# Optimization experiments

Measured on AMD Instinct MI355X. Metric: run time of the kernel, lower is better.

Reference implementation:

```python
import jax, jax.numpy as jnp
import numpy as np

B, S, D = 4, 1024, 1024
H = 16
DH = D // H  # head dim = 64
SCALE = DH ** -0.5
NEG = -1e18


def setup_inputs() -> dict:
    key = jax.random.key(0)
    ks = jax.random.split(key, 8)
    queries = jax.random.normal(ks[0], (B, S, D), dtype=jnp.float32)
    keys_ = jax.random.normal(ks[1], (B, S, D), dtype=jnp.float32)
    values = jax.random.normal(ks[2], (B, S, D), dtype=jnp.float32)
    mask = jax.random.randint(ks[3], (B, 1, S), 0, 2).astype(bool)
    sd = 1.0 / np.sqrt(D)
    Wq = jax.random.normal(ks[4], (D, D), dtype=jnp.float32) * sd
    Wk = jax.random.normal(ks[5], (D, D), dtype=jnp.float32) * sd
    Wv = jax.random.normal(ks[6], (D, D), dtype=jnp.float32) * sd
    Wo = jax.random.normal(ks[7], (D, D), dtype=jnp.float32) * sd
    return {"queries": queries, "keys": keys_, "values": values,
            "Wq": Wq, "Wk": Wk, "Wv": Wv, "Wo": Wo, "mask": mask}


def _split_heads(x):
    # [B,S,D] -> [B,H,S,DH]
    b, s, d = x.shape
    return x.reshape(b, s, H, d // H).transpose(0, 2, 1, 3)


def reference(queries, keys, values, Wq, Wk, Wv, Wo, mask):
    q = _split_heads(queries @ Wq) * SCALE          # [B,H,S,DH]
    k = _split_heads(keys @ Wk)                     # [B,H,S,DH]
    v = _split_heads(values @ Wv)                   # [B,H,S,DH]
    logits = jnp.einsum('bhqd,bhkd->bhqk', q, k)    # [B,H,S,S]
    # mask [B,1,Lk] -> unsqueeze head dim -> broadcast over [B,H,Lq,Lk]
    logits = jnp.where(mask[:, None, :, :], NEG, logits)
    attention_weights = logits.sum(axis=1) / H      # [B,S,S] head-averaged logits
    w = jax.nn.softmax(logits, axis=-1)             # dropout p=0 -> identity
    ctx = jnp.einsum('bhqk,bhkd->bhqd', w, v)       # [B,H,S,DH]
    ctx = ctx.transpose(0, 2, 1, 3).reshape(q.shape[0], q.shape[2], H * DH)
    outputs = ctx @ Wo                              # [B,S,D]
    return (outputs, attention_weights)
```

## Files before the change

### kernel.cpp

```cpp
#include <hip/hip_runtime.h>
#include <hip/hip_bf16.h>

typedef __bf16 bf16;
typedef __attribute__((ext_vector_type(8))) __bf16 bf16x8;
typedef __attribute__((ext_vector_type(4))) __bf16 bf16x4;
typedef __attribute__((ext_vector_type(4))) float f32x4;

#define NEGV (-1e18f)
#define LOG2E 1.4426950408889634f

__device__ __forceinline__ bf16 f2b(float f) {
    unsigned u = __builtin_bit_cast(unsigned, f);
    u += 0x7fffu + ((u >> 16) & 1u);
    unsigned short h = (unsigned short)(u >> 16);
    return __builtin_bit_cast(bf16, h);
}

__device__ __forceinline__ f32x4 mfma16(bf16x8 a, bf16x8 b, f32x4 c) {
    return __builtin_amdgcn_mfma_f32_16x16x32_bf16(a, b, c, 0, 0, 0);
}

__device__ __forceinline__ void gl16(const void* g, void* l) {
    __builtin_amdgcn_global_load_lds((const __attribute__((address_space(1))) void*)g,
                                     (__attribute__((address_space(3))) void*)l, 16, 0, 0);
}

__global__ __launch_bounds__(256) void wconv(const float* __restrict__ W0,
                                             const float* __restrict__ W1,
                                             const float* __restrict__ W2,
                                             const float* __restrict__ W3,
                                             bf16* __restrict__ out) {
    __shared__ float tile[64][65];
    const float* Ws[4] = {W0, W1, W2, W3};
    const float* W = Ws[blockIdx.z];
    bf16* O = out + ((size_t)blockIdx.z << 20);
    int t = threadIdx.x;
    int k0 = blockIdx.x * 64, n0 = blockIdx.y * 64;
#pragma unroll
    for (int p = 0; p < 4; p++) {
        int r = (t >> 4) + p * 16, c = (t & 15) * 4;
        float4 v = *(const float4*)&W[(size_t)(k0 + r) * 1024 + n0 + c];
        tile[r][c] = v.x; tile[r][c + 1] = v.y; tile[r][c + 2] = v.z; tile[r][c + 3] = v.w;
    }
    __syncthreads();
#pragma unroll
    for (int p = 0; p < 4; p++) {
        int r = (t >> 4) + p * 16, c = (t & 15) * 4;
        bf16x4 o;
        o[0] = f2b(tile[c][r]); o[1] = f2b(tile[c + 1][r]);
        o[2] = f2b(tile[c + 2][r]); o[3] = f2b(tile[c + 3][r]);
        *(bf16x4*)&O[(size_t)(n0 + r) * 1024 + k0 + c] = o;
    }
}

__global__ __launch_bounds__(256) void cvt3(const float* __restrict__ Qf,
                                            const float* __restrict__ Kf,
                                            const float* __restrict__ Vf,
                                            bf16* __restrict__ Qa,
                                            bf16* __restrict__ Ka,
                                            bf16* __restrict__ Va) {
    int z = blockIdx.y;
    const float* in = (z == 0) ? Qf : (z == 1) ? Kf : Vf;
    bf16* out = (z == 0) ? Qa : (z == 1) ? Ka : Va;
    size_t i = ((size_t)blockIdx.x * 256 + threadIdx.x) * 8;
    float4 a = *(const float4*)&in[i];
    float4 b = *(const float4*)&in[i + 4];
    bf16x8 o;
    o[0] = f2b(a.x); o[1] = f2b(a.y); o[2] = f2b(a.z); o[3] = f2b(a.w);
    o[4] = f2b(b.x); o[5] = f2b(b.y); o[6] = f2b(b.z); o[7] = f2b(b.w);
    *(bf16x8*)&out[i] = o;
}

__global__ __launch_bounds__(512, 1) void gemm8(const bf16* __restrict__ Qa,
                                                const bf16* __restrict__ Ka,
                                                const bf16* __restrict__ Va,
                                                const bf16* __restrict__ WtQ,
                                                bf16* __restrict__ Qw,
                                                bf16* __restrict__ Kw,
                                                bf16* __restrict__ VtG) {
    __shared__ bf16 LA[2][256 * 64];
    __shared__ bf16 LB[2][256 * 64];
    char* LAB = (char*)LA;
    char* LBB = (char*)LB;
    int t = threadIdx.x;
    int z = blockIdx.z;
    const bf16* A = (z == 0) ? Qa : (z == 1) ? Ka : Va;
    const bf16* Bt = WtQ + ((size_t)z << 20);
    int m0 = blockIdx.x * 256, n0 = blockIdx.y * 256;
    int wid = t >> 6, lane = t & 63;
    int wr = wid >> 2, wc = wid & 3, lr = lane & 15, lg = lane >> 4;
    const int sxl = (lr & 7) << 4;
    const int arow = wr * 128 + lr;
    const int brow = wc * 64 + lr;
    const int c0 = t, c1 = t + 512;
    const int r0 = c0 >> 3, q0 = (c0 & 7) ^ (r0 & 7);
    const int r1 = c1 >> 3, q1 = (c1 & 7) ^ (r1 & 7);

    f32x4 zero = {0.f, 0.f, 0.f, 0.f};
    f32x4 acc[8][4];
#pragma unroll
    for (int m = 0; m < 8; m++)
#pragma unroll
        for (int n = 0; n < 4; n++) acc[m][n] = zero;
    bf16x8 a[4][2], b0[2][2], b1[2][2];

#define STG_A(BUF, HALF, KT)                                                   \
    gl16(&A[(size_t)(m0 + (HALF) * 128 + r0) * 1024 + (KT) * 64 + q0 * 8],     \
         (void*)(LAB + (BUF) * 32768 + (HALF) * 16384 + c0 * 16));             \
    gl16(&A[(size_t)(m0 + (HALF) * 128 + r1) * 1024 + (KT) * 64 + q1 * 8],     \
         (void*)(LAB + (BUF) * 32768 + (HALF) * 16384 + c1 * 16));
#define STG_B(BUF, HALF, KT)                                                   \
    gl16(&Bt[(size_t)(n0 + (HALF) * 128 + r0) * 1024 + (KT) * 64 + q0 * 8],    \
         (void*)(LBB + (BUF) * 32768 + (HALF) * 16384 + c0 * 16));             \
    gl16(&Bt[(size_t)(n0 + (HALF) * 128 + r1) * 1024 + (KT) * 64 + q1 * 8],    \
         (void*)(LBB + (BUF) * 32768 + (HALF) * 16384 + c1 * 16));
#define RD_A(BUF, MH)                                                          \
    {                                                                          \
        _Pragma("unroll") for (int m = 0; m < 4; m++) {                        \
            int row = arow + (MH) * 64 + m * 16;                               \
            _Pragma("unroll") for (int ks = 0; ks < 2; ks++)                   \
                a[m][ks] = *(const bf16x8*)(LAB + (BUF) * 32768 +              \
                           ((row * 128 + ks * 64 + lg * 16) ^ sxl));           \
        }                                                                      \
    }
#define RD_B(BUF, NH, DST)                                                     \
    {                                                                          \
        _Pragma("unroll") for (int n = 0; n < 2; n++) {                        \
            int row = brow + (NH) * 32 + n * 16;                               \
            _Pragma("unroll") for (int ks = 0; ks < 2; ks++)                   \
                DST[n][ks] = *(const bf16x8*)(LBB + (BUF) * 32768 +            \
                             ((row * 128 + ks * 64 + lg * 16) ^ sxl));         \
        }                                                                      \
    }
#define MM(MH, NH, BB)                                                         \
    {                                                                          \
        _Pragma("unroll") for (int m = 0; m < 4; m++)                          \
        _Pragma("unroll") for (int n = 0; n < 2; n++)                          \
        _Pragma("unroll") for (int ks = 0; ks < 2; ks++)                       \
            acc[(MH) * 4 + m][(NH) * 2 + n] =                                  \
                mfma16(a[m][ks], BB[n][ks], acc[(MH) * 4 + m][(NH) * 2 + n]);  \
    }
#define PH_PRE                                                                 \
    __builtin_amdgcn_s_barrier();                                              \
    asm volatile("s_waitcnt lgkmcnt(0)" ::: "memory");                         \
    __builtin_amdgcn_sched_barrier(0);                                         \
    __builtin_amdgcn_s_setprio(1);
#define PH_POST                                                                \
    __builtin_amdgcn_s_setprio(0);                                             \
    __builtin_amdgcn_s_barrier();

    STG_A(0, 0, 0); STG_A(0, 1, 0); STG_B(0, 0, 0); STG_B(0, 1, 0);
    STG_A(1, 0, 1); STG_B(1, 0, 1); STG_B(1, 1, 1);
    asm volatile("s_waitcnt vmcnt(6)" ::: "memory");
    __builtin_amdgcn_s_barrier();

    for (int i = 0; i < 7; i++) {
        int kt = 2 * i;
        RD_A(0, 0); RD_B(0, 0, b0); STG_A(1, 1, kt + 1);
        PH_PRE; MM(0, 0, b0); PH_POST;
        RD_B(0, 1, b1); STG_A(0, 0, kt + 2);
        PH_PRE; MM(0, 1, b1); PH_POST;
        RD_A(0, 1); STG_B(0, 0, kt + 2);
        PH_PRE; MM(1, 0, b0); PH_POST;
        STG_B(0, 1, kt + 2);
        PH_PRE; MM(1, 1, b1);
        __builtin_amdgcn_s_setprio(0);
        asm volatile("s_waitcnt vmcnt(6)" ::: "memory");
        __builtin_amdgcn_s_barrier();
        RD_A(1, 0); RD_B(1, 0, b0); STG_A(0, 1, kt + 2);
        PH_PRE; MM(0, 0, b0); PH_POST;
        RD_B(1, 1, b1); STG_A(1, 0, kt + 3);
        PH_PRE; MM(0, 1, b1); PH_POST;
        RD_A(1, 1); STG_B(1, 0, kt + 3);
        PH_PRE; MM(1, 0, b0); PH_POST;
        STG_B(1, 1, kt + 3);
        PH_PRE; MM(1, 1, b1);
        __builtin_amdgcn_s_setprio(0);
        asm volatile("s_waitcnt vmcnt(6)" ::: "memory");
        __builtin_amdgcn_s_barrier();
    }
    RD_A(0, 0); RD_B(0, 0, b0); STG_A(1, 1, 15);
    PH_PRE; MM(0, 0, b0); PH_POST;
    RD_B(0, 1, b1);
    PH_PRE; MM(0, 1, b1); PH_POST;
    RD_A(0, 1);
    PH_PRE; MM(1, 0, b0); PH_POST;
    PH_PRE; MM(1, 1, b1);
    __builtin_amdgcn_s_setprio(0);
    asm volatile("s_waitcnt vmcnt(0)" ::: "memory");
    __builtin_amdgcn_s_barrier();
    RD_A(1, 0); RD_B(1, 0, b0);
    PH_PRE; MM(0, 0, b0); PH_POST;
    RD_B(1, 1, b1);
    PH_PRE; MM(0, 1, b1); PH_POST;
    RD_A(1, 1);
    PH_PRE; MM(1, 0, b0); PH_POST;
    PH_PRE; MM(1, 1, b1);
    __builtin_amdgcn_s_setprio(0);
#undef STG_A
#undef STG_B
#undef RD_A
#undef RD_B
#undef MM
#undef PH_PRE
#undef PH_POST
#pragma unroll
    for (int m = 0; m < 8; m++) {
        int rowg = m0 + wr * 128 + m * 16 + lg * 4;
#pragma unroll
        for (int n = 0; n < 4; n++) {
            int colg = n0 + wc * 64 + n * 16 + lr;
            if (z == 2) {
                bf16x4 o;
#pragma unroll
                for (int j = 0; j < 4; j++) o[j] = f2b(acc[m][n][j]);
                *(bf16x4*)&VtG[(size_t)colg * 4096 + rowg] = o;
            } else {
                bf16* C = (z == 0) ? Qw : Kw;
                float sc = (z == 0) ? 0.125f : 1.0f;
#pragma unroll
                for (int j = 0; j < 4; j++)
                    C[(size_t)(rowg + j) * 1024 + colg] = f2b(acc[m][n][j] * sc);
            }
        }
    }
}

__global__ __launch_bounds__(256, 3) void gemm_oa(const bf16* __restrict__ CTX,
                                                  const bf16* __restrict__ WtO,
                                                  float* __restrict__ out,
                                                  const bf16* __restrict__ Qw,
                                                  const bf16* __restrict__ Kw,
                                                  float* __restrict__ aw,
                                                  const int* __restrict__ maskp) {
    __shared__ bf16 As[128 * 64];
    __shared__ bf16 Bs[128 * 64];
    char* AsB = (char*)As;
    char* BsB = (char*)Bs;
    int t = threadIdx.x;
    int z = blockIdx.z;
    int bx = blockIdx.x;
    int m0, n0 = blockIdx.y * 128;
    const bf16* A;
    const bf16* Bt;
    float* C;
    const int* mask = nullptr;
    if (z == 0) {
        m0 = bx * 128;
        A = CTX; Bt = WtO; C = out;
    } else {
        int b = bx >> 3;
        m0 = (bx & 7) * 128;
        A = Qw + ((size_t)b << 20); Bt = Kw + ((size_t)b << 20);
        C = aw + ((size_t)b << 20); mask = maskp + b * 1024;
    }
    int wid = t >> 6, lane = t & 63;
    int wr = wid >> 1, wc = wid & 1, lr = lane & 15, lg = lane >> 4;
    f32x4 zero = {0.f, 0.f, 0.f, 0.f};
    f32x4 acc[4][4];
#pragma unroll
    for (int m = 0; m < 4; m++)
#pragma unroll
        for (int n = 0; n < 4; n++) acc[m][n] = zero;

    for (int k0 = 0; k0 < 1024; k0 += 64) {
        __syncthreads();
#pragma unroll
        for (int i = 0; i < 4; i++) {
            int c = wid * 256 + i * 64 + lane;
            int row = c >> 3, q = (c & 7) ^ (row & 7);
            gl16(&A[(size_t)(m0 + row) * 1024 + k0 + q * 8], (void*)&As[c * 8]);
            gl16(&Bt[(size_t)(n0 + row) * 1024 + k0 + q * 8], (void*)&Bs[c * 8]);
        }
        __syncthreads();
#pragma unroll
        for (int kk = 0; kk < 2; kk++) {
            bf16x8 af[4], bfr[4];
#pragma unroll
            for (int m = 0; m < 4; m++) {
                int row = wr * 64 + m * 16 + lr;
                af[m] = *(const bf16x8*)(AsB + ((row * 128 + kk * 64 + lg * 16) ^ ((row & 7) << 4)));
            }
#pragma unroll
            for (int n = 0; n < 4; n++) {
                int row = wc * 64 + n * 16 + lr;
                bfr[n] = *(const bf16x8*)(BsB + ((row * 128 + kk * 64 + lg * 16) ^ ((row & 7) << 4)));
            }
#pragma unroll
            for (int m = 0; m < 4; m++)
#pragma unroll
                for (int n = 0; n < 4; n++) acc[m][n] = mfma16(af[m], bfr[n], acc[m][n]);
        }
    }
#pragma unroll
    for (int n = 0; n < 4; n++) {
        int colg = n0 + wc * 64 + n * 16 + lr;
        int mk = (z == 1) ? mask[colg] : 0;
#pragma unroll
        for (int m = 0; m < 4; m++) {
            int rowg = m0 + wr * 64 + m * 16 + lg * 4;
#pragma unroll
            for (int j = 0; j < 4; j++) {
                float v = acc[m][n][j];
                size_t idx = (size_t)(rowg + j) * 1024 + colg;
                if (z == 0) C[idx] = v;
                else C[idx] = mk ? NEGV : v * (1.f / 16.f);
            }
        }
    }
}

__global__ __launch_bounds__(256, 4) void flash_k(const bf16* __restrict__ Q,
                                                  const bf16* __restrict__ K,
                                                  const bf16* __restrict__ VT,
                                                  bf16* __restrict__ CTX,
                                                  const int* __restrict__ maskp) {
    __shared__ bf16 Ks[64 * 64];
    __shared__ bf16 Vs[64 * 64];
    __shared__ bf16 Ps[4][16 * 64];
    __shared__ float biasS[1024];
    int bid = blockIdx.x;
    int qt = bid & 15, h = (bid >> 4) & 15, b = bid >> 8;
    int t = threadIdx.x, wid = t >> 6, lane = t & 63;
    int lr = lane & 15, lg = lane >> 4;
    int qbase = qt * 64 + wid * 16;
    const size_t bS = (size_t)b * 1024;
    char* KsB = (char*)Ks;
    char* VsB = (char*)Vs;
    char* PsW = (char*)&Ps[wid][0];
    const int sxl = (lr & 7) << 4;

    {
        int4 mv = *(const int4*)&maskp[b * 1024 + t * 4];
        float4 bv;
        const float NB = NEGV * LOG2E;
        bv.x = mv.x ? NB : 0.f; bv.y = mv.y ? NB : 0.f;
        bv.z = mv.z ? NB : 0.f; bv.w = mv.w ? NB : 0.f;
        *(float4*)&biasS[t * 4] = bv;
    }

    bf16x8 qf[2];
#pragma unroll
    for (int c = 0; c < 2; c++)
        qf[c] = *(const bf16x8*)&Q[(bS + qbase + lr) * 1024 + h * 64 + c * 32 + lg * 8];

    f32x4 zero = {0.f, 0.f, 0.f, 0.f};
    f32x4 acc[4];
#pragma unroll
    for (int d = 0; d < 4; d++) acc[d] = zero;
    float mr = -INFINITY;
    float lsum = 0.f;

    const bf16* Kbase = K + bS * 1024 + h * 64;
    const bf16* Vbase = VT + (size_t)(h * 64) * 4096 + bS;

    int c0 = t, c1 = t + 256;
    int kr0 = c0 >> 3, kq0 = c0 & 7, kr1 = c1 >> 3, kq1 = c1 & 7;

    bf16x8 kg[2], vg[2];
    kg[0] = *(const bf16x8*)&Kbase[(size_t)kr0 * 1024 + kq0 * 8];
    kg[1] = *(const bf16x8*)&Kbase[(size_t)kr1 * 1024 + kq1 * 8];
    vg[0] = *(const bf16x8*)&Vbase[(size_t)kr0 * 4096 + kq0 * 8];
    vg[1] = *(const bf16x8*)&Vbase[(size_t)kr1 * 4096 + kq1 * 8];

    for (int kt = 0; kt < 16; kt++) {
        __syncthreads();
        *(bf16x8*)(KsB + ((kr0 * 128 + kq0 * 16) ^ ((kr0 & 7) << 4))) = kg[0];
        *(bf16x8*)(KsB + ((kr1 * 128 + kq1 * 16) ^ ((kr1 & 7) << 4))) = kg[1];
        *(bf16x8*)(VsB + ((kr0 * 128 + kq0 * 16) ^ ((kr0 & 7) << 4))) = vg[0];
        *(bf16x8*)(VsB + ((kr1 * 128 + kq1 * 16) ^ ((kr1 & 7) << 4))) = vg[1];
        __syncthreads();
        if (kt < 15) {
            size_t ko = (size_t)(kt + 1) * 64;
            kg[0] = *(const bf16x8*)&Kbase[(ko + kr0) * 1024 + kq0 * 8];
            kg[1] = *(const bf16x8*)&Kbase[(ko + kr1) * 1024 + kq1 * 8];
            vg[0] = *(const bf16x8*)&Vbase[(size_t)kr0 * 4096 + ko + kq0 * 8];
            vg[1] = *(const bf16x8*)&Vbase[(size_t)kr1 * 4096 + ko + kq1 * 8];
        }
        f32x4 s[4];
        __builtin_amdgcn_s_setprio(1);
#pragma unroll
        for (int n = 0; n < 4; n++) {
            int row = n * 16 + lr;
            bf16x8 kf0 = *(const bf16x8*)(KsB + ((row * 128 + lg * 16) ^ sxl));
            bf16x8 kf1 = *(const bf16x8*)(KsB + ((row * 128 + 64 + lg * 16) ^ sxl));
            f32x4 zz = zero;
            zz = mfma16(kf0, qf[0], zz);
            zz = mfma16(kf1, qf[1], zz);
            s[n] = zz;
        }
        __builtin_amdgcn_s_setprio(0);
#pragma unroll
        for (int n = 0; n < 4; n++) {
            float4 bv = *(const float4*)&biasS[kt * 64 + n * 16 + lg * 4];
            s[n][0] = __builtin_fmaf(s[n][0], LOG2E, bv.x);
            s[n][1] = __builtin_fmaf(s[n][1], LOG2E, bv.y);
            s[n][2] = __builtin_fmaf(s[n][2], LOG2E, bv.z);
            s[n][3] = __builtin_fmaf(s[n][3], LOG2E, bv.w);
        }
        float pm;
        {
            float a0 = fmaxf(fmaxf(s[0][0], s[0][1]), fmaxf(s[0][2], s[0][3]));
            float a1 = fmaxf(fmaxf(s[1][0], s[1][1]), fmaxf(s[1][2], s[1][3]));
            float a2 = fmaxf(fmaxf(s[2][0], s[2][1]), fmaxf(s[2][2], s[2][3]));
            float a3 = fmaxf(fmaxf(s[3][0], s[3][1]), fmaxf(s[3][2], s[3][3]));
            pm = fmaxf(fmaxf(a0, a1), fmaxf(a2, a3));
        }
        pm = fmaxf(pm, __shfl_xor(pm, 16));
        pm = fmaxf(pm, __shfl_xor(pm, 32));
        float mn = fmaxf(mr, pm);
        float sc = __builtin_exp2f(mr - mn);
        mr = mn;
        float rs;
        {
            float r0 = 0.f, r1 = 0.f, r2 = 0.f, r3 = 0.f;
#pragma unroll
            for (int n = 0; n < 4; n++) {
                float p0 = __builtin_exp2f(s[n][0] - mn);
                float p1 = __builtin_exp2f(s[n][1] - mn);
                float p2 = __builtin_exp2f(s[n][2] - mn);
                float p3 = __builtin_exp2f(s[n][3] - mn);
                s[n][0] = p0; s[n][1] = p1; s[n][2] = p2; s[n][3] = p3;
                r0 += p0; r1 += p1; r2 += p2; r3 += p3;
            }
            rs = (r0 + r1) + (r2 + r3);
        }
        rs += __shfl_xor(rs, 16);
        rs += __shfl_xor(rs, 32);
        lsum = lsum * sc + rs;
        float scb[4];
#pragma unroll
        for (int j = 0; j < 4; j++) scb[j] = __shfl(sc, lg * 4 + j);
#pragma unroll
        for (int d = 0; d < 4; d++) {
            acc[d][0] *= scb[0]; acc[d][1] *= scb[1];
            acc[d][2] *= scb[2]; acc[d][3] *= scb[3];
        }
#pragma unroll
        for (int n = 0; n < 4; n++) {
            bf16x4 o;
            o[0] = (bf16)s[n][0]; o[1] = (bf16)s[n][1];
            o[2] = (bf16)s[n][2]; o[3] = (bf16)s[n][3];
            *(bf16x4*)(PsW + ((lr * 128 + n * 32 + lg * 8) ^ sxl)) = o;
        }
        __builtin_amdgcn_s_setprio(1);
#pragma unroll
        for (int c = 0; c < 2; c++) {
            bf16x8 pa = *(const bf16x8*)(PsW + ((lr * 128 + c * 64 + lg * 16) ^ sxl));
#pragma unroll
            for (int d = 0; d < 4; d++) {
                int row = d * 16 + lr;
                bf16x8 vb = *(const bf16x8*)(VsB + ((row * 128 + c * 64 + lg * 16) ^ ((row & 7) << 4)));
                acc[d] = mfma16(pa, vb, acc[d]);
            }
        }
        __builtin_amdgcn_s_setprio(0);
    }
    float lb[4];
#pragma unroll
    for (int j = 0; j < 4; j++) lb[j] = __shfl(lsum, lg * 4 + j);
#pragma unroll
    for (int j = 0; j < 4; j++) {
        float inv = 1.f / lb[j];
#pragma unroll
        for (int d = 0; d < 4; d++)
            CTX[(bS + qbase + lg * 4 + j) * 1024 + h * 64 + d * 16 + lr] = f2b(acc[d][j] * inv);
    }
}

extern "C" void kernel_launch(void* const* d_in, const int* in_sizes, int n_in,
                              void* d_out, int out_size, void* d_ws, size_t ws_size,
                              hipStream_t stream) {
    const float* queries = (const float*)d_in[0];
    const float* keys    = (const float*)d_in[1];
    const float* values  = (const float*)d_in[2];
    const float* Wq = (const float*)d_in[3];
    const float* Wk = (const float*)d_in[4];
    const float* Wv = (const float*)d_in[5];
    const float* Wo = (const float*)d_in[6];
    const int* mask = (const int*)d_in[7];

    float* out = (float*)d_out;
    float* aw  = out + ((size_t)4 << 20);

    bf16* wsb = (bf16*)d_ws;
    bf16* WtQ = wsb;
    bf16* Qa  = wsb + ((size_t)4 << 20);
    bf16* Qw  = wsb + ((size_t)8 << 20);
    bf16* Kw  = wsb + ((size_t)12 << 20);
    bf16* VtG = wsb + ((size_t)16 << 20);
    bf16* Ka  = (bf16*)aw;
    bf16* Va  = (bf16*)aw + ((size_t)4 << 20);
    bf16* CTX = Qa;

    wconv<<<dim3(16, 16, 4), 256, 0, stream>>>(Wq, Wk, Wv, Wo, WtQ);
    cvt3<<<dim3(2048, 3), 256, 0, stream>>>(queries, keys, values, Qa, Ka, Va);
    gemm8<<<dim3(16, 4, 3), 512, 0, stream>>>(Qa, Ka, Va, WtQ, Qw, Kw, VtG);
    flash_k<<<dim3(1024), 256, 0, stream>>>(Qw, Kw, VtG, CTX, mask);
    gemm_oa<<<dim3(32, 8, 2), 256, 0, stream>>>(CTX, WtQ + ((size_t)3 << 20), out,
                                                Qw, Kw, aw, mask);
}
```

Measured before the change: 125.5 us.

## Fuse prep kernels, retune GEMM staging, double-buffer K and lazily rescale softmax

Merges the weight-transpose and activation-convert kernels into one launch to save a launch and its tail. Reorders the A-tile staging in the projection GEMM and waits on vmcnt(4) instead of vmcnt(6). In the flash kernel, K tiles are double-buffered in LDS so a barrier can be dropped, the max reduction uses three-input max, and the online-softmax rescale is skipped unless the running max grows by more than a threshold. The lazy rescale lets exponentials exceed 1 (up to 2^8), which may affect bf16 precision of P. The fused launch mixes two different block workloads.

```diff
diff --git a/kernel.cpp b/kernel.cpp
--- a/kernel.cpp
+++ b/kernel.cpp
@@ -25,17 +25,43 @@
                                      (__attribute__((address_space(3))) void*)l, 16, 0, 0);
 }
 
-__global__ __launch_bounds__(256) void wconv(const float* __restrict__ W0,
-                                             const float* __restrict__ W1,
-                                             const float* __restrict__ W2,
-                                             const float* __restrict__ W3,
-                                             bf16* __restrict__ out) {
+__device__ __forceinline__ float fmax3(float a, float b, float c) {
+    return fmaxf(fmaxf(a, b), c);
+}
+
+__global__ __launch_bounds__(256) void prep(const float* __restrict__ Qf,
+                                            const float* __restrict__ Kf,
+                                            const float* __restrict__ Vf,
+                                            const float* __restrict__ W0,
+                                            const float* __restrict__ W1,
+                                            const float* __restrict__ W2,
+                                            const float* __restrict__ W3,
+                                            bf16* __restrict__ Qa,
+                                            bf16* __restrict__ Ka,
+                                            bf16* __restrict__ Va,
+                                            bf16* __restrict__ Wout) {
     __shared__ float tile[64][65];
+    int bx = blockIdx.x;
+    int t = threadIdx.x;
+    if (bx < 6144) {
+        int z = bx >> 11, x = bx & 2047;
+        const float* in = (z == 0) ? Qf : (z == 1) ? Kf : Vf;
+        bf16* out = (z == 0) ? Qa : (z == 1) ? Ka : Va;
+        size_t i = ((size_t)x * 256 + t) * 8;
+        float4 a = *(const float4*)&in[i];
+        float4 b = *(const float4*)&in[i + 4];
+        bf16x8 o;
+        o[0] = f2b(a.x); o[1] = f2b(a.y); o[2] = f2b(a.z); o[3] = f2b(a.w);
+        o[4] = f2b(b.x); o[5] = f2b(b.y); o[6] = f2b(b.z); o[7] = f2b(b.w);
+        *(bf16x8*)&out[i] = o;
+        return;
+    }
+    int w = bx - 6144;
+    int z = w >> 8;
     const float* Ws[4] = {W0, W1, W2, W3};
-    const float* W = Ws[blockIdx.z];
-    bf16* O = out + ((size_t)blockIdx.z << 20);
-    int t = threadIdx.x;
-    int k0 = blockIdx.x * 64, n0 = blockIdx.y * 64;
+    const float* W = Ws[z];
+    bf16* O = Wout + ((size_t)z << 20);
+    int k0 = (w & 15) * 64, n0 = ((w >> 4) & 15) * 64;
 #pragma unroll
     for (int p = 0; p < 4; p++) {
         int r = (t >> 4) + p * 16, c = (t & 15) * 4;
@@ -51,24 +77,6 @@
         o[2] = f2b(tile[c + 2][r]); o[3] = f2b(tile[c + 3][r]);
         *(bf16x4*)&O[(size_t)(n0 + r) * 1024 + k0 + c] = o;
     }
-}
-
-__global__ __launch_bounds__(256) void cvt3(const float* __restrict__ Qf,
-                                            const float* __restrict__ Kf,
-                                            const float* __restrict__ Vf,
-                                            bf16* __restrict__ Qa,
-                                            bf16* __restrict__ Ka,
-                                            bf16* __restrict__ Va) {
-    int z = blockIdx.y;
-    const float* in = (z == 0) ? Qf : (z == 1) ? Kf : Vf;
-    bf16* out = (z == 0) ? Qa : (z == 1) ? Ka : Va;
-    size_t i = ((size_t)blockIdx.x * 256 + threadIdx.x) * 8;
-    float4 a = *(const float4*)&in[i];
-    float4 b = *(const float4*)&in[i + 4];
-    bf16x8 o;
-    o[0] = f2b(a.x); o[1] = f2b(a.y); o[2] = f2b(a.z); o[3] = f2b(a.w);
-    o[4] = f2b(b.x); o[5] = f2b(b.y); o[6] = f2b(b.z); o[7] = f2b(b.w);
-    *(bf16x8*)&out[i] = o;
 }
 
 __global__ __launch_bounds__(512, 1) void gemm8(const bf16* __restrict__ Qa,
@@ -148,40 +156,38 @@
 #define PH_POST                                                                \
     __builtin_amdgcn_s_setprio(0);                                             \
     __builtin_amdgcn_s_barrier();
+#define VM4_BAR                                                                \
+    __builtin_amdgcn_s_setprio(0);                                             \
+    asm volatile("s_waitcnt vmcnt(4)" ::: "memory");                           \
+    __builtin_amdgcn_s_barrier();
 
     STG_A(0, 0, 0); STG_A(0, 1, 0); STG_B(0, 0, 0); STG_B(0, 1, 0);
-    STG_A(1, 0, 1); STG_B(1, 0, 1); STG_B(1, 1, 1);
-    asm volatile("s_waitcnt vmcnt(6)" ::: "memory");
+    STG_B(1, 0, 1); STG_B(1, 1, 1);
+    asm volatile("s_waitcnt vmcnt(4)" ::: "memory");
     __builtin_amdgcn_s_barrier();
 
     for (int i = 0; i < 7; i++) {
         int kt = 2 * i;
-        RD_A(0, 0); RD_B(0, 0, b0); STG_A(1, 1, kt + 1);
+        RD_A(0, 0); RD_B(0, 0, b0); STG_A(1, 0, kt + 1);
         PH_PRE; MM(0, 0, b0); PH_POST;
-        RD_B(0, 1, b1); STG_A(0, 0, kt + 2);
+        RD_B(0, 1, b1); STG_A(1, 1, kt + 1);
         PH_PRE; MM(0, 1, b1); PH_POST;
         RD_A(0, 1); STG_B(0, 0, kt + 2);
         PH_PRE; MM(1, 0, b0); PH_POST;
         STG_B(0, 1, kt + 2);
-        PH_PRE; MM(1, 1, b1);
-        __builtin_amdgcn_s_setprio(0);
-        asm volatile("s_waitcnt vmcnt(6)" ::: "memory");
-        __builtin_amdgcn_s_barrier();
-        RD_A(1, 0); RD_B(1, 0, b0); STG_A(0, 1, kt + 2);
+        PH_PRE; MM(1, 1, b1); VM4_BAR;
+        RD_A(1, 0); RD_B(1, 0, b0); STG_A(0, 0, kt + 2);
         PH_PRE; MM(0, 0, b0); PH_POST;
-        RD_B(1, 1, b1); STG_A(1, 0, kt + 3);
+        RD_B(1, 1, b1); STG_A(0, 1, kt + 2);
         PH_PRE; MM(0, 1, b1); PH_POST;
         RD_A(1, 1); STG_B(1, 0, kt + 3);
         PH_PRE; MM(1, 0, b0); PH_POST;
         STG_B(1, 1, kt + 3);
-        PH_PRE; MM(1, 1, b1);
-        __builtin_amdgcn_s_setprio(0);
-        asm volatile("s_waitcnt vmcnt(6)" ::: "memory");
-        __builtin_amdgcn_s_barrier();
-    }
-    RD_A(0, 0); RD_B(0, 0, b0); STG_A(1, 1, 15);
+        PH_PRE; MM(1, 1, b1); VM4_BAR;
+    }
+    RD_A(0, 0); RD_B(0, 0, b0); STG_A(1, 0, 15);
     PH_PRE; MM(0, 0, b0); PH_POST;
-    RD_B(0, 1, b1);
+    RD_B(0, 1, b1); STG_A(1, 1, 15);
     PH_PRE; MM(0, 1, b1); PH_POST;
     RD_A(0, 1);
     PH_PRE; MM(1, 0, b0); PH_POST;
@@ -204,6 +210,7 @@
 #undef MM
 #undef PH_PRE
 #undef PH_POST
+#undef VM4_BAR
 #pragma unroll
     for (int m = 0; m < 8; m++) {
         int rowg = m0 + wr * 128 + m * 16 + lg * 4;
@@ -315,7 +322,7 @@
                                                   const bf16* __restrict__ VT,
                                                   bf16* __restrict__ CTX,
                                                   const int* __restrict__ maskp) {
-    __shared__ bf16 Ks[64 * 64];
+    __shared__ bf16 Ks[2][64 * 64];
     __shared__ bf16 Vs[64 * 64];
     __shared__ bf16 Ps[4][16 * 64];
     __shared__ float biasS[1024];
@@ -356,40 +363,51 @@
 
     int c0 = t, c1 = t + 256;
     int kr0 = c0 >> 3, kq0 = c0 & 7, kr1 = c1 >> 3, kq1 = c1 & 7;
-
+    const int kw0 = (kr0 * 128 + kq0 * 16) ^ ((kr0 & 7) << 4);
+    const int kw1 = (kr1 * 128 + kq1 * 16) ^ ((kr1 & 7) << 4);
+
+    {
+        bf16x8 t0 = *(const bf16x8*)&Kbase[(size_t)kr0 * 1024 + kq0 * 8];
+        bf16x8 t1 = *(const bf16x8*)&Kbase[(size_t)kr1 * 1024 + kq1 * 8];
+        *(bf16x8*)(KsB + kw0) = t0;
+        *(bf16x8*)(KsB + kw1) = t1;
+    }
     bf16x8 kg[2], vg[2];
-    kg[0] = *(const bf16x8*)&Kbase[(size_t)kr0 * 1024 + kq0 * 8];
-    kg[1] = *(const bf16x8*)&Kbase[(size_t)kr1 * 1024 + kq1 * 8];
     vg[0] = *(const bf16x8*)&Vbase[(size_t)kr0 * 4096 + kq0 * 8];
     vg[1] = *(const bf16x8*)&Vbase[(size_t)kr1 * 4096 + kq1 * 8];
-
+    kg[0] = *(const bf16x8*)&Kbase[(size_t)(64 + kr0) * 1024 + kq0 * 8];
+    kg[1] = *(const bf16x8*)&Kbase[(size_t)(64 + kr1) * 1024 + kq1 * 8];
+
+    int cur = 0;
     for (int kt = 0; kt < 16; kt++) {
         __syncthreads();
-        *(bf16x8*)(KsB + ((kr0 * 128 + kq0 * 16) ^ ((kr0 & 7) << 4))) = kg[0];
-        *(bf16x8*)(KsB + ((kr1 * 128 + kq1 * 16) ^ ((kr1 & 7) << 4))) = kg[1];
-        *(bf16x8*)(VsB + ((kr0 * 128 + kq0 * 16) ^ ((kr0 & 7) << 4))) = vg[0];
-        *(bf16x8*)(VsB + ((kr1 * 128 + kq1 * 16) ^ ((kr1 & 7) << 4))) = vg[1];
-        __syncthreads();
+        *(bf16x8*)(VsB + kw0) = vg[0];
+        *(bf16x8*)(VsB + kw1) = vg[1];
         if (kt < 15) {
+            *(bf16x8*)(KsB + (cur ^ 1) * 8192 + kw0) = kg[0];
+            *(bf16x8*)(KsB + (cur ^ 1) * 8192 + kw1) = kg[1];
             size_t ko = (size_t)(kt + 1) * 64;
-            kg[0] = *(const bf16x8*)&Kbase[(ko + kr0) * 1024 + kq0 * 8];
-            kg[1] = *(const bf16x8*)&Kbase[(ko + kr1) * 1024 + kq1 * 8];
             vg[0] = *(const bf16x8*)&Vbase[(size_t)kr0 * 4096 + ko + kq0 * 8];
             vg[1] = *(const bf16x8*)&Vbase[(size_t)kr1 * 4096 + ko + kq1 * 8];
+            if (kt < 14) {
+                kg[0] = *(const bf16x8*)&Kbase[(ko + 64 + kr0) * 1024 + kq0 * 8];
+                kg[1] = *(const bf16x8*)&Kbase[(ko + 64 + kr1) * 1024 + kq1 * 8];
+            }
         }
         f32x4 s[4];
         __builtin_amdgcn_s_setprio(1);
 #pragma unroll
         for (int n = 0; n < 4; n++) {
             int row = n * 16 + lr;
-            bf16x8 kf0 = *(const bf16x8*)(KsB + ((row * 128 + lg * 16) ^ sxl));
-            bf16x8 kf1 = *(const bf16x8*)(KsB + ((row * 128 + 64 + lg * 16) ^ sxl));
+            bf16x8 kf0 = *(const bf16x8*)(KsB + cur * 8192 + ((row * 128 + lg * 16) ^ sxl));
+            bf16x8 kf1 = *(const bf16x8*)(KsB + cur * 8192 + ((row * 128 + 64 + lg * 16) ^ sxl));
             f32x4 zz = zero;
             zz = mfma16(kf0, qf[0], zz);
             zz = mfma16(kf1, qf[1], zz);
             s[n] = zz;
         }
         __builtin_amdgcn_s_setprio(0);
+        __syncthreads();
 #pragma unroll
         for (int n = 0; n < 4; n++) {
             float4 bv = *(const float4*)&biasS[kt * 64 + n * 16 + lg * 4];
@@ -400,26 +418,38 @@
         }
         float pm;
         {
-            float a0 = fmaxf(fmaxf(s[0][0], s[0][1]), fmaxf(s[0][2], s[0][3]));
-            float a1 = fmaxf(fmaxf(s[1][0], s[1][1]), fmaxf(s[1][2], s[1][3]));
-            float a2 = fmaxf(fmaxf(s[2][0], s[2][1]), fmaxf(s[2][2], s[2][3]));
-            float a3 = fmaxf(fmaxf(s[3][0], s[3][1]), fmaxf(s[3][2], s[3][3]));
-            pm = fmaxf(fmaxf(a0, a1), fmaxf(a2, a3));
+            float t1 = fmax3(s[0][0], s[0][1], s[0][2]);
+            float t2 = fmax3(s[0][3], s[1][0], s[1][1]);
+            float t3 = fmax3(s[1][2], s[1][3], s[2][0]);
+            float t4 = fmax3(s[2][1], s[2][2], s[2][3]);
+            float t5 = fmax3(s[3][0], s[3][1], s[3][2]);
+            pm = fmax3(fmax3(t1, t2, t3), fmax3(t4, t5, s[3][3]), -INFINITY);
         }
         pm = fmaxf(pm, __shfl_xor(pm, 16));
         pm = fmaxf(pm, __shfl_xor(pm, 32));
-        float mn = fmaxf(mr, pm);
-        float sc = __builtin_exp2f(mr - mn);
-        mr = mn;
+        if (!__all(pm <= mr + 8.f)) {
+            float mn = fmaxf(mr, pm);
+            float sc = __builtin_exp2f(mr - mn);
+            mr = mn;
+            lsum *= sc;
+            float scb[4];
+#pragma unroll
+            for (int j = 0; j < 4; j++) scb[j] = __shfl(sc, lg * 4 + j);
+#pragma unroll
+            for (int d = 0; d < 4; d++) {
+                acc[d][0] *= scb[0]; acc[d][1] *= scb[1];
+                acc[d][2] *= scb[2]; acc[d][3] *= scb[3];
+            }
+        }
         float rs;
         {
             float r0 = 0.f, r1 = 0.f, r2 = 0.f, r3 = 0.f;
 #pragma unroll
             for (int n = 0; n < 4; n++) {
-                float p0 = __builtin_exp2f(s[n][0] - mn);
-                float p1 = __builtin_exp2f(s[n][1] - mn);
-                float p2 = __builtin_exp2f(s[n][2] - mn);
-                float p3 = __builtin_exp2f(s[n][3] - mn);
+                float p0 = __builtin_exp2f(s[n][0] - mr);
+                float p1 = __builtin_exp2f(s[n][1] - mr);
+                float p2 = __builtin_exp2f(s[n][2] - mr);
+                float p3 = __builtin_exp2f(s[n][3] - mr);
                 s[n][0] = p0; s[n][1] = p1; s[n][2] = p2; s[n][3] = p3;
                 r0 += p0; r1 += p1; r2 += p2; r3 += p3;
             }
@@ -427,15 +457,7 @@
         }
         rs += __shfl_xor(rs, 16);
         rs += __shfl_xor(rs, 32);
-        lsum = lsum * sc + rs;
-        float scb[4];
-#pragma unroll
-        for (int j = 0; j < 4; j++) scb[j] = __shfl(sc, lg * 4 + j);
-#pragma unroll
-        for (int d = 0; d < 4; d++) {
-            acc[d][0] *= scb[0]; acc[d][1] *= scb[1];
-            acc[d][2] *= scb[2]; acc[d][3] *= scb[3];
-        }
+        lsum += rs;
 #pragma unroll
         for (int n = 0; n < 4; n++) {
             bf16x4 o;
@@ -455,6 +477,7 @@
             }
         }
         __builtin_amdgcn_s_setprio(0);
+        cur ^= 1;
     }
     float lb[4];
 #pragma unroll
@@ -493,8 +516,8 @@
     bf16* Va  = (bf16*)aw + ((size_t)4 << 20);
     bf16* CTX = Qa;
 
-    wconv<<<dim3(16, 16, 4), 256, 0, stream>>>(Wq, Wk, Wv, Wo, WtQ);
-    cvt3<<<dim3(2048, 3), 256, 0, stream>>>(queries, keys, values, Qa, Ka, Va);
+    prep<<<dim3(7168), 256, 0, stream>>>(queries, keys, values, Wq, Wk, Wv, Wo,
+                                         Qa, Ka, Va, WtQ);
     gemm8<<<dim3(16, 4, 3), 512, 0, stream>>>(Qa, Ka, Va, WtQ, Qw, Kw, VtG);
     flash_k<<<dim3(1024), 256, 0, stream>>>(Qw, Kw, VtG, CTX, mask);
     gemm_oa<<<dim3(32, 8, 2), 256, 0, stream>>>(CTX, WtQ + ((size_t)3 << 20), out,
```

After: 122.1 us. 1.03x faster.
